# Optimization experiments

Measured on AMD Instinct MI355X. Metric: run time of the kernel, lower is better.

The kernel has to match this reference:

```python
import jax, jax.numpy as jnp
import numpy as np
from jax.scipy.linalg import expm
jax.config.update("jax_enable_x64", True)

HBAR = 0.6582119569
CM2EV = 0.00012398419
N6A, N10A = 4, 4
DT = 1.0
KDC = dict(E_S1=3.995, E_S2=4.9183, om6a=596.0 * CM2EV, om10a=919.0 * CM2EV,
           kap6a_S1=-0.0964, kap6a_S2=0.1193, lam=0.1825, gamma=-0.018)


def _build():
    cd = np.complex128

    def ladder(n):
        a = np.zeros((n, n), dtype=cd)
        for k in range(1, n):
            a[k - 1, k] = np.sqrt(float(k))
        adag = a.conj().T
        return (a + adag) / np.sqrt(2.0), adag @ a, np.eye(n, dtype=cd)

    Q6a1, N6a1, I6a = ladder(N6A)
    Q10a1, N10a1, I10a = ladder(N10A)
    Nel, Dvib = 3, N6A * N10A
    Ivib = np.eye(Dvib, dtype=cd)
    Iel = np.eye(Nel, dtype=cd)
    lift = lambda op: np.kron(Iel, op)
    Q6a = lift(np.kron(Q6a1, I10a))
    Q10a = lift(np.kron(I6a, Q10a1))
    N6a = lift(np.kron(N6a1, I10a))
    N10a = lift(np.kron(I6a, N10a1))
    P = []
    for k in range(Nel):
        ek = np.zeros(Nel, dtype=cd); ek[k] = 1.0
        P.append(np.kron(np.outer(ek, ek), Ivib))
    e1 = np.zeros(Nel, dtype=cd); e1[1] = 1.0
    e2 = np.zeros(Nel, dtype=cd); e2[2] = 1.0
    Poff = np.kron(np.outer(e1, e2) + np.outer(e2, e1), Ivib)
    Lj = np.kron(np.outer(e1, e2), Ivib)  # |S1><S2| lift
    D = Nel * Dvib
    I = np.eye(D, dtype=cd)
    p = KDC
    H = (p['E_S1'] * P[1] + p['E_S2'] * P[2] + p['om6a'] * N6a + p['om10a'] * N10a
         + p['kap6a_S1'] * P[1] @ Q6a + p['kap6a_S2'] * P[2] @ Q6a
         + p['lam'] * Poff @ Q10a + p['gamma'] * Poff @ (Q10a @ Q10a))
    # Coherent part -i(I kron H - H^T* kron I); dissipator at unit rate (scaled by g later)
    Lc = -1j * (np.kron(I, H) - np.kron(H.conj().T, I))
    LdL = Lj.conj().T @ Lj
    Ld0 = (np.kron(Lj.conj(), Lj) - 0.5 * np.kron(I, LdL)
           - 0.5 * np.kron(LdL.conj().T, I))
    psi = np.zeros(D, dtype=cd); psi[2 * N6A * N10A] = 1.0
    rho0 = np.outer(psi, psi.conj()).reshape(-1)
    trP = np.stack([P[k].T.reshape(-1) for k in range(3)])  # [3, D^2]
    return Lc, Ld0, rho0, trP

_LC, _LD0, _RHO0, _TRP = _build()


def setup_inputs() -> dict:
    return {"log_g": jnp.asarray(np.log(1.0 / 40.0), dtype=jnp.float32),
            "n_steps": 1000}


def reference(log_g, n_steps):
    Lc = jnp.asarray(_LC)
    Ld0 = jnp.asarray(_LD0)
    rho0 = jnp.asarray(_RHO0)
    trP = jnp.asarray(_TRP)
    g = jnp.exp(log_g).astype(jnp.float64)
    Lsup = Lc + g * Ld0                      # [D^2, D^2] complex128
    U = expm(Lsup * (DT / HBAR))             # one-step propagator

    def step(rho, _):
        pops = jnp.real(trP @ rho)           # tr(P_k rho), k=0..2
        return U @ rho, pops

    _, ps = jax.lax.scan(step, rho0, None, length=int(n_steps))  # [n_steps, 3]
    return (ps[:, 0].astype(jnp.float32),
            ps[:, 1].astype(jnp.float32),
            ps[:, 2].astype(jnp.float32))
```

## Files before the change

### kernel.cpp

```cpp
#include <hip/hip_runtime.h>
#include <math.h>


#define DS 1024
#define MATD ((size_t)DS * DS * sizeof(double))
#define PA 66

typedef double v4d __attribute__((ext_vector_type(4)));

__device__ inline double Qel(int i, int j) {
    if (i == j + 1) return sqrt((double)i) * 0.70710678118654752440;
    if (j == i + 1) return sqrt((double)j) * 0.70710678118654752440;
    return 0.0;
}

__device__ inline void fill_H(double* Hs, int tid) {
    const double CM2EV = 0.00012398419;
    const double E_S1 = 3.995, E_S2 = 4.9183;
    const double om6a = 596.0 * CM2EV, om10a = 919.0 * CM2EV;
    const double kapA = -0.0964, kapB = 0.1193, lam = 0.1825, gam = -0.018;
    for (int h = tid; h < 1024; h += 256) {
        int r = h >> 5, c = h & 31;
        int e = r >> 4, v6 = (r >> 2) & 3, v10 = r & 3;
        int e2 = c >> 4, w6 = (c >> 2) & 3, w10 = c & 3;
        double val = 0.0;
        if (r == c) val += (e ? E_S2 : E_S1) + om6a * v6 + om10a * v10;
        if (e == e2 && v10 == w10) val += (e ? kapB : kapA) * Qel(v6, w6);
        if (e != e2 && v6 == w6) {
            double q2 = 0.0;
            #pragma unroll
            for (int m = 0; m < 4; ++m) q2 += Qel(v10, m) * Qel(m, w10);
            val += lam * Qel(v10, w10) + gam * q2;
        }
        Hs[h] = val;
    }
}

__global__ __launch_bounds__(256)
void build_G10(const float* __restrict__ logg, double* __restrict__ X,
               double* __restrict__ Y, double* __restrict__ Z)
{
    int tid = threadIdx.x;
    if (blockIdx.x >= 4096) {
        int idx = (blockIdx.x - 4096) * 256 + tid;
        if (idx < 64 * 1024) {
            int r = idx >> 10, i = idx & 1023;
            double v = 0.0;
            if (r < 2 && i % 33 == 0) {
                int a = i / 33;
                if ((a < 16) == (r == 0)) v = 1.0;
            }
            Y[idx] = v;
        } else if (idx < 64 * 1024 + 1024) {
            int i = idx - 64 * 1024;
            Z[i] = (i == 528) ? 1.0 : 0.0;
        }
        return;
    }
    __shared__ double Hs[1024];
    fill_H(Hs, tid);
    __syncthreads();
    double g = exp((double)logg[0]);
    const double sc = ((1.0 / 0.6582119569) / 16.0) / 10.0;
    int idx = blockIdx.x * 256 + tid;
    int r = idx >> 10, c = idx & 1023;
    int i = r >> 5, j = r & 31;
    int k = c >> 5, l = c & 31;
    double t = 0.0;
    if (k <= l) {
        if (i <= j) {
            if (i < 16 && j < 16) {
                int p = i + 16, q = j + 16;
                if ((p == k && q == l) || (p == l && q == k)) t += g;
            }
            if (i == k && j == l) t -= 0.5 * g * ((i >= 16) + (j >= 16));
        } else {
            if (j == l) t += Hs[i * 32 + k];
            if (k != l && j == k) t += Hs[i * 32 + l];
            if (i == k) t -= Hs[l * 32 + j];
            if (k != l && i == l) t -= Hs[k * 32 + j];
        }
    } else {
        if (i <= j) {
            double ha = 0.0;
            if (j == l) ha += Hs[i * 32 + k];
            if (j == k) ha -= Hs[i * 32 + l];
            if (i == k) ha -= Hs[l * 32 + j];
            if (i == l) ha += Hs[k * 32 + j];
            t -= ha;
        } else {
            if (i < 16 && j < 16 && (i + 16 == k) && (j + 16 == l)) t += g;
            if (i == k && j == l) t -= 0.5 * g * ((i >= 16) + (j >= 16));
        }
    }
    X[idx] = t * sc + ((r == c) ? 1.0 : 0.0);
}

__global__ __launch_bounds__(256)
void apply_T(const float* __restrict__ logg, const double* __restrict__ M,
             double* __restrict__ O, double invk)
{
    __shared__ double Hs[1024];
    __shared__ int    qlist[120];
    __shared__ double wl[4][120];
    __shared__ int    counts[4];
    __shared__ int    Kshared;
    const int tid = threadIdx.x;
    fill_H(Hs, tid);
    __syncthreads();
    const double g = exp((double)logg[0]);
    const double sck = ((1.0 / 0.6582119569) / 16.0) * invk;

    const int sw = ((blockIdx.x & 7) << 7) | (blockIdx.x >> 3);
    const int grp = sw >> 2, q4 = sw & 3;
    const int a = grp >> 4, b = grp & 15;
    const int i0 = a << 1, j0 = b << 1;
    const int wv = tid >> 6, lane = tid & 63;
    const int m = lane & 31;

    bool valid = false; int q = 0;
    double w0 = 0.0, w1 = 0.0, w2 = 0.0, w3 = 0.0;

    if (a != b) {
        if (lane < 32) {
            const bool fam2 = (wv >= 2);
            const int sel = wv & 1;
            if (!fam2) {
                const int js = j0 + sel;
                double cA = Hs[i0 * 32 + m];
                double cB = Hs[(i0 + 1) * 32 + m];
                if (a < b) {
                    if ((cA != 0.0 || cB != 0.0) && m != js) {
                        valid = true;
                        q = (m > js) ? m * 32 + js : js * 32 + m;
                        double sA = (m > js) ? -cA : cA;
                        double sB = (m > js) ? -cB : cB;
                        if (sel == 0) { w0 = sA; w2 = sB; }
                        else          { w1 = sA; w3 = sB; }
                    }
                } else {
                    if (cA != 0.0 || cB != 0.0) {
                        valid = true;
                        q = (m < js) ? m * 32 + js : js * 32 + m;
                        if (sel == 0) { w0 = cA; w2 = cB; }
                        else          { w1 = cA; w3 = cB; }
                    }
                }
            } else {
                const int is = i0 + sel;
                double c0 = Hs[m * 32 + j0];
                double c1 = Hs[m * 32 + j0 + 1];
                if (a < b) {
                    if ((c0 != 0.0 || c1 != 0.0) && m != is) {
                        valid = true;
                        q = (is > m) ? is * 32 + m : m * 32 + is;
                        double s0 = (is > m) ? c0 : -c0;
                        double s1 = (is > m) ? c1 : -c1;
                        if (sel == 0) { w0 = s0; w1 = s1; }
                        else          { w2 = s0; w3 = s1; }
                    }
                } else {
                    if (c0 != 0.0 || c1 != 0.0) {
                        valid = true;
                        q = (m < is) ? m * 32 + is : is * 32 + m;
                        if (sel == 0) { w0 = -c0; w1 = -c1; }
                        else          { w2 = -c0; w3 = -c1; }
                    }
                }
            }
        }
    } else {
        const int ia = i0 + (wv >> 1), ja = j0 + (wv & 1);
        const bool up = (ia <= ja);
        double wr = 0.0;
        if (lane < 32) {
            double c = Hs[ia * 32 + m];
            if (up) {
                if (c != 0.0 && m != ja) {
                    valid = true;
                    q = (m > ja) ? m * 32 + ja : ja * 32 + m;
                    wr = (m > ja) ? -c : c;
                }
            } else {
                if (c != 0.0) {
                    valid = true;
                    q = (m < ja) ? m * 32 + ja : ja * 32 + m;
                    wr = c;
                }
            }
        } else {
            double c = Hs[m * 32 + ja];
            if (up) {
                if (c != 0.0 && m != ia) {
                    valid = true;
                    q = (ia > m) ? ia * 32 + m : m * 32 + ia;
                    wr = (ia > m) ? c : -c;
                }
            } else {
                if (c != 0.0) {
                    valid = true;
                    q = (m < ia) ? m * 32 + ia : ia * 32 + m;
                    wr = -c;
                }
            }
        }
        if (wv == 0) w0 = wr; else if (wv == 1) w1 = wr;
        else if (wv == 2) w2 = wr; else w3 = wr;
    }

    unsigned long long mask = __ballot(valid);
    if (lane == 0) counts[wv] = __popcll(mask);
    __syncthreads();
    int base = 0;
    for (int t = 0; t < wv; ++t) base += counts[t];
    if (valid) {
        int slot = base + __popcll(mask & ((1ull << lane) - 1ull));
        qlist[slot] = q;
        wl[0][slot] = w0; wl[1][slot] = w1; wl[2][slot] = w2; wl[3][slot] = w3;
    }
    __syncthreads();
    if (tid == 0) {
        int K = counts[0] + counts[1] + counts[2] + counts[3];
        const int cnt = (a >= 8) + (b >= 8);
        if (a < 8 && b < 8) {
            #pragma unroll
            for (int r = 0; r < 4; ++r) {
                int ia = i0 + (r >> 1), ja = j0 + (r & 1);
                qlist[K] = (ia + 16) * 32 + (ja + 16);
                wl[0][K] = 0.0; wl[1][K] = 0.0; wl[2][K] = 0.0; wl[3][K] = 0.0;
                wl[r][K] = g; ++K;
            }
        }
        if (cnt > 0) {
            double wd = -0.5 * g * (double)cnt;
            #pragma unroll
            for (int r = 0; r < 4; ++r) {
                int ia = i0 + (r >> 1), ja = j0 + (r & 1);
                qlist[K] = ia * 32 + ja;
                wl[0][K] = 0.0; wl[1][K] = 0.0; wl[2][K] = 0.0; wl[3][K] = 0.0;
                wl[r][K] = wd; ++K;
            }
        }
        while (K & 7) {
            qlist[K] = 0;
            wl[0][K] = 0.0; wl[1][K] = 0.0; wl[2][K] = 0.0; wl[3][K] = 0.0;
            ++K;
        }
        Kshared = K;
    }
    __syncthreads();
    const int K = Kshared;

    const int col = (q4 << 8) + tid;
    double a0 = 0.0, a1 = 0.0, a2 = 0.0, a3 = 0.0;
    for (int k = 0; k < K; k += 8) {
        #pragma unroll
        for (int u = 0; u < 8; ++u) {
            int qq = qlist[k + u];
            double v = M[(size_t)qq * DS + col];
            a0 += wl[0][k + u] * v;
            a1 += wl[1][k + u] * v;
            a2 += wl[2][k + u] * v;
            a3 += wl[3][k + u] * v;
        }
    }

    double accs[4] = {a0, a1, a2, a3};
    #pragma unroll
    for (int r = 0; r < 4; ++r) {
        int pr = (i0 + (r >> 1)) * 32 + (j0 + (r & 1));
        O[(size_t)pr * DS + col] = sck * accs[r] + ((pr == col) ? 1.0 : 0.0);
    }
}

__global__ __launch_bounds__(1024, 1)
void dgemm(const double* __restrict__ A, const double* __restrict__ B,
           double* __restrict__ D)
{
    __shared__ double As[2][64 * PA];
    __shared__ double Bs[2][64 * PA];
    const int tid = threadIdx.x;
    const int bm = blockIdx.x << 6, bn = blockIdx.y << 6;
    const int w = tid >> 6, lane = tid & 63;
    const int lr = lane & 15, lk = lane >> 4;
    const int p = w & 3, kg = w >> 2;
    const int wr = (p >> 1) << 5, wc = (p & 1) << 5;

    v4d acc[2][2];
    #pragma unroll
    for (int si = 0; si < 2; ++si)
        #pragma unroll
        for (int sj = 0; sj < 2; ++sj) acc[si][sj] = (v4d){0., 0., 0., 0.};

    const int ra = tid >> 4;
    const int cs = (tid & 15) << 2;
    const double* gA = A + (size_t)(bm + ra) * DS + cs;
    const double* gB = B + (size_t)ra * DS + bn + cs;
    double va[4], vb[4];
    #pragma unroll
    for (int u = 0; u < 4; ++u) { va[u] = gA[u]; vb[u] = gB[u]; }
    #pragma unroll
    for (int u = 0; u < 4; ++u) {
        As[0][ra * PA + cs + u] = va[u];
        Bs[0][ra * PA + cs + u] = vb[u];
    }
    #pragma unroll
    for (int u = 0; u < 4; ++u) {
        va[u] = gA[64 + u];
        vb[u] = gB[(size_t)64 * DS + u];
    }
    __syncthreads();

    #pragma unroll 2
    for (int kt = 0; kt < DS; kt += 64) {
        const int pb = (kt >> 6) & 1;
        const bool more  = (kt + 64) < DS;
        const bool more2 = (kt + 128) < DS;
        const int k0 = (kg << 4) + lk;
        double A00 = As[pb][(wr + lr) * PA + k0];
        double A10 = As[pb][(wr + 16 + lr) * PA + k0];
        double B00 = Bs[pb][k0 * PA + wc + lr];
        double B10 = Bs[pb][k0 * PA + wc + 16 + lr];
        double A01 = As[pb][(wr + lr) * PA + k0 + 4];
        double A11 = As[pb][(wr + 16 + lr) * PA + k0 + 4];
        double B01 = Bs[pb][(k0 + 4) * PA + wc + lr];
        double B11 = Bs[pb][(k0 + 4) * PA + wc + 16 + lr];
        acc[0][0] = __builtin_amdgcn_mfma_f64_16x16x4f64(A00, B00, acc[0][0], 0, 0, 0);
        acc[0][1] = __builtin_amdgcn_mfma_f64_16x16x4f64(A00, B10, acc[0][1], 0, 0, 0);
        acc[1][0] = __builtin_amdgcn_mfma_f64_16x16x4f64(A10, B00, acc[1][0], 0, 0, 0);
        acc[1][1] = __builtin_amdgcn_mfma_f64_16x16x4f64(A10, B10, acc[1][1], 0, 0, 0);
        acc[0][0] = __builtin_amdgcn_mfma_f64_16x16x4f64(A01, B01, acc[0][0], 0, 0, 0);
        acc[0][1] = __builtin_amdgcn_mfma_f64_16x16x4f64(A01, B11, acc[0][1], 0, 0, 0);
        acc[1][0] = __builtin_amdgcn_mfma_f64_16x16x4f64(A11, B01, acc[1][0], 0, 0, 0);
        acc[1][1] = __builtin_amdgcn_mfma_f64_16x16x4f64(A11, B11, acc[1][1], 0, 0, 0);
        if (more) {
            #pragma unroll
            for (int u = 0; u < 4; ++u) {
                As[pb ^ 1][ra * PA + cs + u] = va[u];
                Bs[pb ^ 1][ra * PA + cs + u] = vb[u];
            }
        }
        if (more2) {
            #pragma unroll
            for (int u = 0; u < 4; ++u) {
                va[u] = gA[kt + 128 + u];
                vb[u] = gB[(size_t)(kt + 128) * DS + u];
            }
        }
        double A02 = As[pb][(wr + lr) * PA + k0 + 8];
        double A12 = As[pb][(wr + 16 + lr) * PA + k0 + 8];
        double B02 = Bs[pb][(k0 + 8) * PA + wc + lr];
        double B12 = Bs[pb][(k0 + 8) * PA + wc + 16 + lr];
        double A03 = As[pb][(wr + lr) * PA + k0 + 12];
        double A13 = As[pb][(wr + 16 + lr) * PA + k0 + 12];
        double B03 = Bs[pb][(k0 + 12) * PA + wc + lr];
        double B13 = Bs[pb][(k0 + 12) * PA + wc + 16 + lr];
        acc[0][0] = __builtin_amdgcn_mfma_f64_16x16x4f64(A02, B02, acc[0][0], 0, 0, 0);
        acc[0][1] = __builtin_amdgcn_mfma_f64_16x16x4f64(A02, B12, acc[0][1], 0, 0, 0);
        acc[1][0] = __builtin_amdgcn_mfma_f64_16x16x4f64(A12, B02, acc[1][0], 0, 0, 0);
        acc[1][1] = __builtin_amdgcn_mfma_f64_16x16x4f64(A12, B12, acc[1][1], 0, 0, 0);
        acc[0][0] = __builtin_amdgcn_mfma_f64_16x16x4f64(A03, B03, acc[0][0], 0, 0, 0);
        acc[0][1] = __builtin_amdgcn_mfma_f64_16x16x4f64(A03, B13, acc[0][1], 0, 0, 0);
        acc[1][0] = __builtin_amdgcn_mfma_f64_16x16x4f64(A13, B03, acc[1][0], 0, 0, 0);
        acc[1][1] = __builtin_amdgcn_mfma_f64_16x16x4f64(A13, B13, acc[1][1], 0, 0, 0);
        __syncthreads();
    }

    double* red = &As[0][0];
    if (kg == 3) {
        #pragma unroll
        for (int si = 0; si < 2; ++si)
            #pragma unroll
            for (int sj = 0; sj < 2; ++sj)
                #pragma unroll
                for (int r = 0; r < 4; ++r)
                    red[(wr + si * 16 + lk + 4 * r) * 64 + wc + sj * 16 + lr]
                        = acc[si][sj][r];
    }
    __syncthreads();
    if (kg == 2) {
        #pragma unroll
        for (int si = 0; si < 2; ++si)
            #pragma unroll
            for (int sj = 0; sj < 2; ++sj)
                #pragma unroll
                for (int r = 0; r < 4; ++r)
                    red[(wr + si * 16 + lk + 4 * r) * 64 + wc + sj * 16 + lr]
                        += acc[si][sj][r];
    }
    __syncthreads();
    if (kg == 1) {
        #pragma unroll
        for (int si = 0; si < 2; ++si)
            #pragma unroll
            for (int sj = 0; sj < 2; ++sj)
                #pragma unroll
                for (int r = 0; r < 4; ++r)
                    red[(wr + si * 16 + lk + 4 * r) * 64 + wc + sj * 16 + lr]
                        += acc[si][sj][r];
    }
    __syncthreads();
    if (kg == 0) {
        #pragma unroll
        for (int si = 0; si < 2; ++si)
            #pragma unroll
            for (int sj = 0; sj < 2; ++sj) {
                int col = bn + wc + sj * 16 + lr;
                #pragma unroll
                for (int r = 0; r < 4; ++r) {
                    int row = bm + wr + si * 16 + lk + 4 * r;
                    D[(size_t)row * DS + col] = acc[si][sj][r]
                        + red[(wr + si * 16 + lk + 4 * r) * 64 + wc + sj * 16 + lr];
                }
            }
    }
}

__global__ __launch_bounds__(256)
void ypart(const double* __restrict__ P, const double* __restrict__ Y,
           double* __restrict__ scratch, int SR)
{
    __shared__ double Yld[32 * 64];
    __shared__ double red[32 * 64];
    const int tid = threadIdx.x;
    const int cc = tid & 63, kw = tid >> 6;
    const int col = (blockIdx.x << 6) + cc;
    const int kb = blockIdx.y << 6;
    const int r0 = blockIdx.z << 5;

    for (int idx = tid; idx < 32 * 64; idx += 256) {
        int r = idx >> 6, kk = idx & 63;
        Yld[idx] = Y[(size_t)(r0 + r) * DS + kb + kk];
    }
    __syncthreads();

    double acc[32];
    #pragma unroll
    for (int r = 0; r < 32; ++r) acc[r] = 0.0;

    #pragma unroll
    for (int kk = 0; kk < 16; ++kk) {
        int kl = (kw << 4) + kk;
        double pv = P[(size_t)(kb + kl) * DS + col];
        #pragma unroll
        for (int r = 0; r < 32; ++r)
            acc[r] += Yld[(r << 6) + kl] * pv;
    }

    __syncthreads();
    if (kw == 3) {
        #pragma unroll
        for (int r = 0; r < 32; ++r) red[(r << 6) + cc] = acc[r];
    }
    __syncthreads();
    if (kw == 2) {
        #pragma unroll
        for (int r = 0; r < 32; ++r) red[(r << 6) + cc] += acc[r];
    }
    __syncthreads();
    if (kw == 1) {
        #pragma unroll
        for (int r = 0; r < 32; ++r) red[(r << 6) + cc] += acc[r];
    }
    __syncthreads();
    if (kw == 0) {
        #pragma unroll
        for (int r = 0; r < 32; ++r) red[(r << 6) + cc] += acc[r];
    }
    __syncthreads();
    for (int idx = tid; idx < 32 * 64; idx += 256) {
        int r = idx >> 6, c2 = idx & 63;
        scratch[((size_t)blockIdx.y * SR + r0 + r) * DS + (blockIdx.x << 6) + c2]
            = red[idx];
    }
}

__global__ __launch_bounds__(256)
void yreduce(const double* __restrict__ scratch, double* __restrict__ Y,
             int M, int SR)
{
    int idx = blockIdx.x * 256 + threadIdx.x;
    int r = idx >> 10, c = idx & 1023;
    double s = 0.0;
    #pragma unroll
    for (int q = 0; q < 16; ++q)
        s += scratch[((size_t)q * SR + r) * DS + c];
    Y[(size_t)(M + r) * DS + c] = s;
}

__global__ __launch_bounds__(256)
void zstep(const double* __restrict__ V, const double* __restrict__ Zin,
           double* __restrict__ Zout)
{
    int row = blockIdx.x * 4 + (threadIdx.x >> 6);
    int lane = threadIdx.x & 63;
    const double2* r_ = (const double2*)(V + (size_t)row * DS);
    const double2* z_ = (const double2*)Zin;
    double s = 0.0;
    #pragma unroll
    for (int k = 0; k < 8; ++k) {
        double2 a = r_[(k << 6) + lane];
        double2 b = z_[(k << 6) + lane];
        s += a.x * b.x + a.y * b.y;
    }
    #pragma unroll
    for (int off = 32; off; off >>= 1) s += __shfl_down(s, off);
    if (lane == 0) Zout[row] = s;
}

__global__ __launch_bounds__(128)
void final_pops(const double* __restrict__ Y, const double* __restrict__ Z,
                float* __restrict__ out, int n)
{
    int t = blockIdx.x;
    int k = threadIdx.x >> 6, lane = threadIdx.x & 63;
    int a = t & 31, j = t >> 5;
    const double* y = Y + (size_t)(2 * a + k) * 1024;
    const double* z = Z + (size_t)j * 1024;
    double s = 0.0;
    for (int i = lane; i < 1024; i += 64) s += y[i] * z[i];
    #pragma unroll
    for (int off = 32; off; off >>= 1) s += __shfl_down(s, off);
    if (lane == 0) {
        out[(size_t)(k + 1) * n + t] = (float)s;
        if (k == 0) out[t] = 0.0f;
    }
}

static inline void ydouble2(const double* P, double* Y, double* scr, int M,
                            hipStream_t stream)
{
    int gz = (M + 31) / 32; if (gz < 1) gz = 1;
    int SR = gz * 32;
    ypart<<<dim3(16, 16, gz), 256, 0, stream>>>(P, Y, scr, SR);
    yreduce<<<SR * 4, 256, 0, stream>>>(scr, Y, M, SR);
}

extern "C" void kernel_launch(void* const* d_in, const int* in_sizes, int n_in,
                              void* d_out, int out_size, void* d_ws, size_t ws_size,
                              hipStream_t stream)
{
    const float* logg = (const float*)d_in[0];
    float* out = (float*)d_out;
    const int n = out_size / 3;
    (void)in_sizes; (void)n_in; (void)ws_size;

    char* ws = (char*)d_ws;
    double* b0 = (double*)(ws + 0 * MATD);
    double* b1 = (double*)(ws + 1 * MATD);
    double* b2 = (double*)(ws + 2 * MATD);
    double* scr = (double*)(ws + 3 * MATD);
    double* Y  = (double*)(ws + 5 * MATD);
    double* Z  = Y + 64 * 1024;

    dim3 g2(16, 16);

    build_G10<<<4096 + 260, 256, 0, stream>>>(logg, b0, Y, Z);
    double* src = b0; double* dst = b1;
    for (int k = 9; k >= 1; --k) {
        apply_T<<<1024, 256, 0, stream>>>(logg, src, dst, 1.0 / (double)k);
        double* t = src; src = dst; dst = t;
    }

    dgemm<<<g2, 1024, 0, stream>>>(b1, b1, b0);
    dgemm<<<g2, 1024, 0, stream>>>(b0, b0, b2);
    dgemm<<<g2, 1024, 0, stream>>>(b2, b2, b1);
    dgemm<<<g2, 1024, 0, stream>>>(b1, b1, b0);
    ydouble2(b0, Y, scr, 2, stream);
    dgemm<<<g2, 1024, 0, stream>>>(b0, b0, b1);
    ydouble2(b1, Y, scr, 4, stream);
    dgemm<<<g2, 1024, 0, stream>>>(b1, b1, b2);
    ydouble2(b2, Y, scr, 8, stream);
    dgemm<<<g2, 1024, 0, stream>>>(b2, b2, b1);
    ydouble2(b1, Y, scr, 16, stream);
    dgemm<<<g2, 1024, 0, stream>>>(b1, b1, b2);
    ydouble2(b2, Y, scr, 32, stream);
    dgemm<<<g2, 1024, 0, stream>>>(b2, b2, b1);

    for (int j = 1; j < 32; ++j)
        zstep<<<256, 256, 0, stream>>>(b1, Z + (size_t)(j - 1) * 1024,
                                       Z + (size_t)j * 1024);

    final_pops<<<n, 128, 0, stream>>>(Y, Z, out, n);
}
```

Baseline: 644.2 us.

## Replace split-K dgemm with 32x64-tile single-accumulator kernel on more blocks

Rewrites the 1024x1024 FP64 squaring GEMM. Each block now computes a 32x64 output tile with 8 waves, and each wave owns one 16x16 MFMA accumulator over the full K. This removes the 4-way split-K and its shared-memory reduction, and the grid doubles to 512 blocks so more CUs have work. In exchange the LDS double buffering is dropped in favour of a single buffer with two barriers per K tile. Each wave also reuses less data per LDS load, since one A and one B fragment feed one MFMA instead of four.

After: 757.8 us. 1.18x slower.

```diff
diff --git a/kernel.cpp b/kernel.cpp
--- a/kernel.cpp
+++ b/kernel.cpp
@@ -273,146 +273,61 @@
     }
 }
 
-__global__ __launch_bounds__(1024, 1)
+__global__ __launch_bounds__(512, 2)
 void dgemm(const double* __restrict__ A, const double* __restrict__ B,
            double* __restrict__ D)
 {
-    __shared__ double As[2][64 * PA];
-    __shared__ double Bs[2][64 * PA];
+    __shared__ double As[32 * PA];
+    __shared__ double Bs[64 * PA];
     const int tid = threadIdx.x;
-    const int bm = blockIdx.x << 6, bn = blockIdx.y << 6;
+    const int bm = blockIdx.x << 5, bn = blockIdx.y << 6;
     const int w = tid >> 6, lane = tid & 63;
     const int lr = lane & 15, lk = lane >> 4;
-    const int p = w & 3, kg = w >> 2;
-    const int wr = (p >> 1) << 5, wc = (p & 1) << 5;
-
-    v4d acc[2][2];
-    #pragma unroll
-    for (int si = 0; si < 2; ++si)
-        #pragma unroll
-        for (int sj = 0; sj < 2; ++sj) acc[si][sj] = (v4d){0., 0., 0., 0.};
-
-    const int ra = tid >> 4;
-    const int cs = (tid & 15) << 2;
-    const double* gA = A + (size_t)(bm + ra) * DS + cs;
-    const double* gB = B + (size_t)ra * DS + bn + cs;
-    double va[4], vb[4];
-    #pragma unroll
-    for (int u = 0; u < 4; ++u) { va[u] = gA[u]; vb[u] = gB[u]; }
-    #pragma unroll
-    for (int u = 0; u < 4; ++u) {
-        As[0][ra * PA + cs + u] = va[u];
-        Bs[0][ra * PA + cs + u] = vb[u];
-    }
-    #pragma unroll
-    for (int u = 0; u < 4; ++u) {
-        va[u] = gA[64 + u];
-        vb[u] = gB[(size_t)64 * DS + u];
-    }
-    __syncthreads();
-
-    #pragma unroll 2
+    const int tr = w >> 2, tc = w & 3;
+
+    v4d acc = (v4d){0., 0., 0., 0.};
+
+    const int arow = tid >> 4, ak0 = (tid & 15) << 2;
+    const int bk = tid >> 3, bc0 = (tid & 7) << 3;
+    const double* gA = A + (size_t)(bm + arow) * DS + ak0;
+    const double* gB = B + (size_t)bk * DS + bn + bc0;
+    double va[4], vb[8];
+    #pragma unroll
+    for (int u = 0; u < 4; ++u) va[u] = gA[u];
+    #pragma unroll
+    for (int u = 0; u < 8; ++u) vb[u] = gB[u];
+
+    const int abase = (tr << 4) * PA;
+    const int bbase = (tc << 4) + lr;
+
     for (int kt = 0; kt < DS; kt += 64) {
-        const int pb = (kt >> 6) & 1;
-        const bool more  = (kt + 64) < DS;
-        const bool more2 = (kt + 128) < DS;
-        const int k0 = (kg << 4) + lk;
-        double A00 = As[pb][(wr + lr) * PA + k0];
-        double A10 = As[pb][(wr + 16 + lr) * PA + k0];
-        double B00 = Bs[pb][k0 * PA + wc + lr];
-        double B10 = Bs[pb][k0 * PA + wc + 16 + lr];
-        double A01 = As[pb][(wr + lr) * PA + k0 + 4];
-        double A11 = As[pb][(wr + 16 + lr) * PA + k0 + 4];
-        double B01 = Bs[pb][(k0 + 4) * PA + wc + lr];
-        double B11 = Bs[pb][(k0 + 4) * PA + wc + 16 + lr];
-        acc[0][0] = __builtin_amdgcn_mfma_f64_16x16x4f64(A00, B00, acc[0][0], 0, 0, 0);
-        acc[0][1] = __builtin_amdgcn_mfma_f64_16x16x4f64(A00, B10, acc[0][1], 0, 0, 0);
-        acc[1][0] = __builtin_amdgcn_mfma_f64_16x16x4f64(A10, B00, acc[1][0], 0, 0, 0);
-        acc[1][1] = __builtin_amdgcn_mfma_f64_16x16x4f64(A10, B10, acc[1][1], 0, 0, 0);
-        acc[0][0] = __builtin_amdgcn_mfma_f64_16x16x4f64(A01, B01, acc[0][0], 0, 0, 0);
-        acc[0][1] = __builtin_amdgcn_mfma_f64_16x16x4f64(A01, B11, acc[0][1], 0, 0, 0);
-        acc[1][0] = __builtin_amdgcn_mfma_f64_16x16x4f64(A11, B01, acc[1][0], 0, 0, 0);
-        acc[1][1] = __builtin_amdgcn_mfma_f64_16x16x4f64(A11, B11, acc[1][1], 0, 0, 0);
-        if (more) {
+        __syncthreads();
+        #pragma unroll
+        for (int u = 0; u < 4; ++u) As[arow * PA + ak0 + u] = va[u];
+        #pragma unroll
+        for (int u = 0; u < 8; ++u) Bs[bk * PA + bc0 + u] = vb[u];
+        __syncthreads();
+        if (kt + 64 < DS) {
             #pragma unroll
-            for (int u = 0; u < 4; ++u) {
-                As[pb ^ 1][ra * PA + cs + u] = va[u];
-                Bs[pb ^ 1][ra * PA + cs + u] = vb[u];
-            }
-        }
-        if (more2) {
+            for (int u = 0; u < 4; ++u) va[u] = gA[kt + 64 + u];
             #pragma unroll
-            for (int u = 0; u < 4; ++u) {
-                va[u] = gA[kt + 128 + u];
-                vb[u] = gB[(size_t)(kt + 128) * DS + u];
-            }
-        }
-        double A02 = As[pb][(wr + lr) * PA + k0 + 8];
-        double A12 = As[pb][(wr + 16 + lr) * PA + k0 + 8];
-        double B02 = Bs[pb][(k0 + 8) * PA + wc + lr];
-        double B12 = Bs[pb][(k0 + 8) * PA + wc + 16 + lr];
-        double A03 = As[pb][(wr + lr) * PA + k0 + 12];
-        double A13 = As[pb][(wr + 16 + lr) * PA + k0 + 12];
-        double B03 = Bs[pb][(k0 + 12) * PA + wc + lr];
-        double B13 = Bs[pb][(k0 + 12) * PA + wc + 16 + lr];
-        acc[0][0] = __builtin_amdgcn_mfma_f64_16x16x4f64(A02, B02, acc[0][0], 0, 0, 0);
-        acc[0][1] = __builtin_amdgcn_mfma_f64_16x16x4f64(A02, B12, acc[0][1], 0, 0, 0);
-        acc[1][0] = __builtin_amdgcn_mfma_f64_16x16x4f64(A12, B02, acc[1][0], 0, 0, 0);
-        acc[1][1] = __builtin_amdgcn_mfma_f64_16x16x4f64(A12, B12, acc[1][1], 0, 0, 0);
-        acc[0][0] = __builtin_amdgcn_mfma_f64_16x16x4f64(A03, B03, acc[0][0], 0, 0, 0);
-        acc[0][1] = __builtin_amdgcn_mfma_f64_16x16x4f64(A03, B13, acc[0][1], 0, 0, 0);
-        acc[1][0] = __builtin_amdgcn_mfma_f64_16x16x4f64(A13, B03, acc[1][0], 0, 0, 0);
-        acc[1][1] = __builtin_amdgcn_mfma_f64_16x16x4f64(A13, B13, acc[1][1], 0, 0, 0);
-        __syncthreads();
-    }
-
-    double* red = &As[0][0];
-    if (kg == 3) {
-        #pragma unroll
-        for (int si = 0; si < 2; ++si)
-            #pragma unroll
-            for (int sj = 0; sj < 2; ++sj)
-                #pragma unroll
-                for (int r = 0; r < 4; ++r)
-                    red[(wr + si * 16 + lk + 4 * r) * 64 + wc + sj * 16 + lr]
-                        = acc[si][sj][r];
-    }
-    __syncthreads();
-    if (kg == 2) {
-        #pragma unroll
-        for (int si = 0; si < 2; ++si)
-            #pragma unroll
-            for (int sj = 0; sj < 2; ++sj)
-                #pragma unroll
-                for (int r = 0; r < 4; ++r)
-                    red[(wr + si * 16 + lk + 4 * r) * 64 + wc + sj * 16 + lr]
-                        += acc[si][sj][r];
-    }
-    __syncthreads();
-    if (kg == 1) {
-        #pragma unroll
-        for (int si = 0; si < 2; ++si)
-            #pragma unroll
-            for (int sj = 0; sj < 2; ++sj)
-                #pragma unroll
-                for (int r = 0; r < 4; ++r)
-                    red[(wr + si * 16 + lk + 4 * r) * 64 + wc + sj * 16 + lr]
-                        += acc[si][sj][r];
-    }
-    __syncthreads();
-    if (kg == 0) {
-        #pragma unroll
-        for (int si = 0; si < 2; ++si)
-            #pragma unroll
-            for (int sj = 0; sj < 2; ++sj) {
-                int col = bn + wc + sj * 16 + lr;
-                #pragma unroll
-                for (int r = 0; r < 4; ++r) {
-                    int row = bm + wr + si * 16 + lk + 4 * r;
-                    D[(size_t)row * DS + col] = acc[si][sj][r]
-                        + red[(wr + si * 16 + lk + 4 * r) * 64 + wc + sj * 16 + lr];
-                }
-            }
+            for (int u = 0; u < 8; ++u)
+                vb[u] = gB[(size_t)(kt + 64) * DS + u];
+        }
+        #pragma unroll
+        for (int s = 0; s < 16; ++s) {
+            const int k = (s << 2) + lk;
+            double av = As[abase + lr * PA + k];
+            double bv = Bs[k * PA + bbase];
+            acc = __builtin_amdgcn_mfma_f64_16x16x4f64(av, bv, acc, 0, 0, 0);
+        }
+    }
+
+    const int col = bn + (tc << 4) + lr;
+    #pragma unroll
+    for (int r = 0; r < 4; ++r) {
+        const int row = bm + (tr << 4) + lk + (r << 2);
+        D[(size_t)row * DS + col] = acc[r];
     }
 }
 
@@ -553,7 +468,7 @@
     double* Y  = (double*)(ws + 5 * MATD);
     double* Z  = Y + 64 * 1024;
 
-    dim3 g2(16, 16);
+    dim3 g2(32, 16);
 
     build_G10<<<4096 + 260, 256, 0, stream>>>(logg, b0, Y, Z);
     double* src = b0; double* dst = b1;
@@ -562,20 +477,20 @@
         double* t = src; src = dst; dst = t;
     }
 
-    dgemm<<<g2, 1024, 0, stream>>>(b1, b1, b0);
-    dgemm<<<g2, 1024, 0, stream>>>(b0, b0, b2);
-    dgemm<<<g2, 1024, 0, stream>>>(b2, b2, b1);
-    dgemm<<<g2, 1024, 0, stream>>>(b1, b1, b0);
+    dgemm<<<g2, 512, 0, stream>>>(b1, b1, b0);
+    dgemm<<<g2, 512, 0, stream>>>(b0, b0, b2);
+    dgemm<<<g2, 512, 0, stream>>>(b2, b2, b1);
+    dgemm<<<g2, 512, 0, stream>>>(b1, b1, b0);
     ydouble2(b0, Y, scr, 2, stream);
-    dgemm<<<g2, 1024, 0, stream>>>(b0, b0, b1);
+    dgemm<<<g2, 512, 0, stream>>>(b0, b0, b1);
     ydouble2(b1, Y, scr, 4, stream);
-    dgemm<<<g2, 1024, 0, stream>>>(b1, b1, b2);
+    dgemm<<<g2, 512, 0, stream>>>(b1, b1, b2);
     ydouble2(b2, Y, scr, 8, stream);
-    dgemm<<<g2, 1024, 0, stream>>>(b2, b2, b1);
+    dgemm<<<g2, 512, 0, stream>>>(b2, b2, b1);
     ydouble2(b1, Y, scr, 16, stream);
-    dgemm<<<g2, 1024, 0, stream>>>(b1, b1, b2);
+    dgemm<<<g2, 512, 0, stream>>>(b1, b1, b2);
     ydouble2(b2, Y, scr, 32, stream);
-    dgemm<<<g2, 1024, 0, stream>>>(b2, b2, b1);
+    dgemm<<<g2, 512, 0, stream>>>(b2, b2, b1);
 
     for (int j = 1; j < 32; ++j)
         zstep<<<256, 256, 0, stream>>>(b1, Z + (size_t)(j - 1) * 1024,
```
